# Kernel optimization log

Hardware: AMD Instinct MI355X
Metric: run time of the kernel (lower is better)

Reference implementation:

```python
import jax, jax.numpy as jnp
import numpy as np

N_EMBD = 1024
N_HEAD = 16
HEAD_DIM = N_EMBD // N_HEAD
B, T = 2, 2048
EPS = 1e-5


def _layernorm(x, gamma, beta):
    mu = jnp.mean(x, axis=-1, keepdims=True)
    var = jnp.mean((x - mu) ** 2, axis=-1, keepdims=True)
    return gamma * (x - mu) / jnp.sqrt(var + EPS) + beta


def setup_inputs() -> dict:
    key = jax.random.key(0)
    ks = jax.random.split(key, 12)
    s = 0.02
    d, f = N_EMBD, 4 * N_EMBD
    return {
        "x": jax.random.normal(ks[0], (B, T, d), dtype=jnp.float32),
        "ln1_g": jnp.ones((d,), jnp.float32),
        "ln1_b": jnp.zeros((d,), jnp.float32),
        "wq": jax.random.normal(ks[1], (d, d), jnp.float32) * s,
        "bq": jnp.zeros((d,), jnp.float32),
        "wk": jax.random.normal(ks[2], (d, d), jnp.float32) * s,
        "bk": jnp.zeros((d,), jnp.float32),
        "wv": jax.random.normal(ks[3], (d, d), jnp.float32) * s,
        "bv": jnp.zeros((d,), jnp.float32),
        "wo": jax.random.normal(ks[4], (d, d), jnp.float32) * s,
        "bo": jnp.zeros((d,), jnp.float32),
        "ln2_g": jnp.ones((d,), jnp.float32),
        "ln2_b": jnp.zeros((d,), jnp.float32),
        "w1": jax.random.normal(ks[5], (d, f), jnp.float32) * s,
        "b1": jnp.zeros((f,), jnp.float32),
        "w2": jax.random.normal(ks[6], (f, d), jnp.float32) * s,
        "b2": jnp.zeros((d,), jnp.float32),
    }


def reference(x, ln1_g, ln1_b, wq, bq, wk, bk, wv, bv, wo, bo,
              ln2_g, ln2_b, w1, b1, w2, b2):
    Bn, Tn, C = x.shape
    # --- attention branch (dropout = identity, eval mode) ---
    xn = _layernorm(x, ln1_g, ln1_b)
    q = (xn @ wq + bq).reshape(Bn, Tn, N_HEAD, HEAD_DIM)
    k = (xn @ wk + bk).reshape(Bn, Tn, N_HEAD, HEAD_DIM)
    v = (xn @ wv + bv).reshape(Bn, Tn, N_HEAD, HEAD_DIM)
    scale = 1.0 / jnp.sqrt(jnp.float32(HEAD_DIM))
    scores = jnp.einsum("bqhd,bkhd->bhqk", q, k) * scale  # [B,H,T,T]
    causal = jnp.tril(jnp.ones((Tn, Tn), dtype=bool))
    scores = jnp.where(causal[None, None], scores, -jnp.inf)
    weights = jax.nn.softmax(scores, axis=-1)
    attn = jnp.einsum("bhqk,bkhd->bqhd", weights, v).reshape(Bn, Tn, C)
    x = x + (attn @ wo + bo)
    # --- MLP branch ---
    h = _layernorm(x, ln2_g, ln2_b)
    h = jax.nn.gelu(h @ w1 + b1, approximate=False)
    x = x + (h @ w2 + b2)
    return x
```

## Files before the change

### kernel.cpp

```cpp
#include <hip/hip_runtime.h>
#include <stdint.h>

#define T_SEQ 2048
#define NHEAD 16
#define HDIM 64
#define CDIM 1024
#define FDIM 4096
#define MROWS 4096
#define NQB 32
#define SMAX 8.0f

typedef __bf16 bf16;
typedef __bf16 bf16x8 __attribute__((ext_vector_type(8)));
typedef float f32x4 __attribute__((ext_vector_type(4)));

__device__ __forceinline__ void gload_lds16(const void* g, void* l) {
  __builtin_amdgcn_global_load_lds(
      (const __attribute__((address_space(1))) void*)g,
      (__attribute__((address_space(3))) void*)l, 16, 0, 0);
}

__device__ __forceinline__ float gelu_tanh(float v) {
  float u = 0.7978845608f * (v + 0.044715f * v * v * v);
  float e = exp2f(u * 2.885390082f);
  float th = 1.0f - 2.0f / (e + 1.0f);
  return 0.5f * v * (1.0f + th);
}

__device__ __forceinline__ void wt_body(const float* __restrict__ src,
                                        bf16* __restrict__ dst, int K, int N,
                                        int k0, int n0) {
  __shared__ float tile[64][65];
  int tid = threadIdx.x;
  int r4 = tid >> 4, c4 = (tid & 15) * 4;
#pragma unroll
  for (int p = 0; p < 4; ++p) {
    int r = p * 16 + r4;
    float4 v = *(const float4*)&src[(size_t)(k0 + r) * N + n0 + c4];
    tile[r][c4] = v.x; tile[r][c4 + 1] = v.y;
    tile[r][c4 + 2] = v.z; tile[r][c4 + 3] = v.w;
  }
  __syncthreads();
  int n8 = tid >> 3, k8 = (tid & 7) * 8;
#pragma unroll
  for (int p = 0; p < 2; ++p) {
    int n = p * 32 + n8;
    union { bf16 h[8]; uint4 u; } t;
#pragma unroll
    for (int j = 0; j < 8; ++j) t.h[j] = (bf16)tile[k8 + j][n];
    *(uint4*)&dst[(size_t)(n0 + n) * K + k0 + k8] = t.u;
  }
}

__global__ void wt_kernel(const float* __restrict__ src, bf16* __restrict__ dst,
                          int K, int N) {
  wt_body(src, dst, K, N, blockIdx.y * 64, blockIdx.x * 64);
}

__global__ void wt4_kernel(const float* s0, const float* s1, const float* s2,
                           const float* s3, bf16* d0, bf16* d1, bf16* d2, bf16* d3) {
  const float* src = blockIdx.z == 0 ? s0 : blockIdx.z == 1 ? s1 : blockIdx.z == 2 ? s2 : s3;
  bf16* dst = blockIdx.z == 0 ? d0 : blockIdx.z == 1 ? d1 : blockIdx.z == 2 ? d2 : d3;
  wt_body(src, dst, 1024, 1024, blockIdx.y * 64, blockIdx.x * 64);
}

__global__ void vt_kernel(const bf16* __restrict__ v, bf16* __restrict__ vt) {
  __shared__ bf16 tile[64][65];
  int bh = blockIdx.y;
  int t0 = blockIdx.x * 64;
  int tid = threadIdx.x;
  const bf16* src = v + (size_t)bh * T_SEQ * HDIM;
  bf16* dst = vt + (size_t)bh * HDIM * T_SEQ;
  int r8 = tid >> 3, c8 = (tid & 7) * 8;
#pragma unroll
  for (int p = 0; p < 2; ++p) {
    int r = p * 32 + r8;
    union { uint4 u; bf16 h[8]; } t;
    t.u = *(const uint4*)&src[(size_t)(t0 + r) * HDIM + c8];
#pragma unroll
    for (int j = 0; j < 8; ++j) tile[r][c8 + j] = t.h[j];
  }
  __syncthreads();
#pragma unroll
  for (int p = 0; p < 2; ++p) {
    int d = p * 32 + r8;
    union { uint4 u; bf16 h[8]; } t;
#pragma unroll
    for (int j = 0; j < 8; ++j) t.h[j] = tile[c8 + j][d];
    *(uint4*)&dst[(size_t)d * T_SEQ + t0 + c8] = t.u;
  }
}

__global__ __launch_bounds__(256)
void ln_kernel(const float* __restrict__ x, const float* __restrict__ g,
               const float* __restrict__ b, bf16* __restrict__ out) {
  int row = blockIdx.x;
  int tid = threadIdx.x;
  float4 v = *(const float4*)&x[(size_t)row * CDIM + tid * 4];
  float s = v.x + v.y + v.z + v.w;
  float ss = v.x * v.x + v.y * v.y + v.z * v.z + v.w * v.w;
#pragma unroll
  for (int off = 1; off < 64; off <<= 1) {
    s += __shfl_xor(s, off, 64);
    ss += __shfl_xor(ss, off, 64);
  }
  __shared__ float red[8];
  int wv = tid >> 6, ln = tid & 63;
  if (ln == 0) { red[wv] = s; red[4 + wv] = ss; }
  __syncthreads();
  s = red[0] + red[1] + red[2] + red[3];
  ss = red[4] + red[5] + red[6] + red[7];
  float mu = s * (1.0f / CDIM);
  float var = ss * (1.0f / CDIM) - mu * mu;
  float rstd = rsqrtf(var + 1e-5f);
  float4 gv = *(const float4*)&g[tid * 4];
  float4 bv = *(const float4*)&b[tid * 4];
  union { bf16 h[4]; uint2 u; } o;
  o.h[0] = (bf16)(gv.x * (v.x - mu) * rstd + bv.x);
  o.h[1] = (bf16)(gv.y * (v.y - mu) * rstd + bv.y);
  o.h[2] = (bf16)(gv.z * (v.z - mu) * rstd + bv.z);
  o.h[3] = (bf16)(gv.w * (v.w - mu) * rstd + bv.w);
  *(uint2*)&out[(size_t)row * CDIM + tid * 4] = o.u;
}

__global__ __launch_bounds__(256)
void addp_kernel(float* __restrict__ out, const float* __restrict__ p1, int n4) {
  int i = blockIdx.x * 256 + threadIdx.x;
  int stride = gridDim.x * 256;
  for (; i < n4; i += stride) {
    f32x4 a = *(const f32x4*)&out[i * 4];
    f32x4 b = *(const f32x4*)&p1[i * 4];
    a += b;
    *(f32x4*)&out[i * 4] = a;
  }
}

enum { EPI_QKV = 0, EPI_F32RES = 1, EPI_GELU = 2, EPI_SPLIT = 3 };

template <int EPI, int BN>
__global__ __launch_bounds__(512, 1)
void gemm256(const bf16* __restrict__ A, const bf16* __restrict__ Bt,
             const float* __restrict__ bias, const float* __restrict__ bias2,
             const float* __restrict__ bias3, const float* res,
             void* outp, void* out2, void* out3, int M, int N, int K, int Kstride) {
  constexpr int WCOLS = BN / 64;
  constexpr int WROWS = 8 / WCOLS;
  constexpr int MR = (256 / WROWS) / 16;
  constexpr int MH = MR / 2;
  constexpr int BCH = BN / 128;
  __shared__ __align__(16) bf16 As[3][256 * 32];
  __shared__ __align__(16) bf16 Bs[3][BN * 32];
  int tid = threadIdx.x;
  int w = tid >> 6, l = tid & 63;
  int wr = w / WCOLS, wc = w % WCOLS;
  int lo = l & 15, g = l >> 4;

  int nwg = gridDim.x * gridDim.y;
  int orig = blockIdx.y * gridDim.x + blockIdx.x;
  int lid = (orig & 7) * (nwg >> 3) + (orig >> 3);
  int bx = lid % gridDim.x, by = lid / gridDim.x;
  int m0 = by * 256, n0 = bx * BN;
  int koff = blockIdx.z * K;

  f32x4 acc[MR][4];
#pragma unroll
  for (int i = 0; i < MR; ++i)
#pragma unroll
    for (int j = 0; j < 4; ++j) acc[i][j] = (f32x4){0.f, 0.f, 0.f, 0.f};

  const bf16* Ab = A + (size_t)m0 * Kstride + koff;
  const bf16* Bb = Bt + (size_t)n0 * Kstride + koff;

  int srow = tid >> 2;
  int scol = ((tid & 3) ^ ((tid >> 3) & 3)) * 8;
  auto STAGE_A = [&](int t, int buf) {
    int k0 = t * 32;
#pragma unroll
    for (int c = 0; c < 2; ++c)
      gload_lds16(Ab + (size_t)(c * 128 + srow) * Kstride + k0 + scol,
                  &As[buf][c * 4096 + w * 512]);
  };
  auto STAGE_B = [&](int t, int buf) {
    int k0 = t * 32;
#pragma unroll
    for (int c = 0; c < BCH; ++c)
      gload_lds16(Bb + (size_t)(c * 128 + srow) * Kstride + k0 + scol,
                  &Bs[buf][c * 4096 + w * 512]);
  };

  int nt = K >> 5;
  STAGE_A(0, 0); STAGE_B(0, 0);
  STAGE_A(1, 1); STAGE_B(1, 1);
  if constexpr (BN == 256) asm volatile("s_waitcnt vmcnt(4)" ::: "memory");
  else                     asm volatile("s_waitcnt vmcnt(3)" ::: "memory");
  __syncthreads();
  int sw = (lo >> 1) & 3;
  int b0 = 0;
  for (int t = 0; t < nt; ++t) {
    int b2 = b0 - 1; if (b2 < 0) b2 += 3;
    bf16x8 af[MH], bfr[4];
#pragma unroll
    for (int m = 0; m < MH; ++m) {
      int R = wr * (MR * 16) + m * 16 + lo;
      af[m] = *(const bf16x8*)&As[b0][R * 32 + (g ^ sw) * 8];
    }
#pragma unroll
    for (int n = 0; n < 4; ++n) {
      int R = wc * 64 + n * 16 + lo;
      bfr[n] = *(const bf16x8*)&Bs[b0][R * 32 + (g ^ sw) * 8];
    }
    if (t + 2 < nt) STAGE_A(t + 2, b2);
    asm volatile("s_barrier" ::: "memory");
    __builtin_amdgcn_s_setprio(1);
#pragma unroll
    for (int m = 0; m < MH; ++m)
#pragma unroll
      for (int n = 0; n < 4; ++n)
        acc[m][n] = __builtin_amdgcn_mfma_f32_16x16x32_bf16(af[m], bfr[n], acc[m][n], 0, 0, 0);
    __builtin_amdgcn_s_setprio(0);
#pragma unroll
    for (int m = 0; m < MH; ++m) {
      int R = wr * (MR * 16) + (m + MH) * 16 + lo;
      af[m] = *(const bf16x8*)&As[b0][R * 32 + (g ^ sw) * 8];
    }
    if (t + 2 < nt) {
      STAGE_B(t + 2, b2);
      if constexpr (BN == 256) asm volatile("s_waitcnt vmcnt(4)" ::: "memory");
      else                     asm volatile("s_waitcnt vmcnt(3)" ::: "memory");
    } else if (t + 1 < nt) {
      asm volatile("s_waitcnt vmcnt(0)" ::: "memory");
    }
    asm volatile("s_barrier" ::: "memory");
    __builtin_amdgcn_s_setprio(1);
#pragma unroll
    for (int m = 0; m < MH; ++m)
#pragma unroll
      for (int n = 0; n < 4; ++n)
        acc[m + MH][n] = __builtin_amdgcn_mfma_f32_16x16x32_bf16(af[m], bfr[n], acc[m + MH][n], 0, 0, 0);
    __builtin_amdgcn_s_setprio(0);
    b0 = (b0 == 2) ? 0 : b0 + 1;
  }

  if constexpr (EPI == EPI_QKV) {
    int which = n0 >> 10;
    const float* bb = which == 0 ? bias : (which == 1 ? bias2 : bias3);
    bf16* ob = (bf16*)(which == 0 ? outp : (which == 1 ? out2 : out3));
#pragma unroll
    for (int m = 0; m < MR; ++m)
#pragma unroll
      for (int n = 0; n < 4; ++n)
#pragma unroll
        for (int j = 0; j < 4; ++j) {
          int row = m0 + wr * (MR * 16) + m * 16 + g * 4 + j;
          int col = n0 + wc * 64 + n * 16 + lo;
          int cw = col & (CDIM - 1);
          float v = acc[m][n][j] + bb[cw];
          int b = row >> 11, tt = row & (T_SEQ - 1);
          int h = cw >> 6, d = cw & (HDIM - 1);
          ob[(((size_t)(b * NHEAD + h)) * T_SEQ + tt) * HDIM + d] = (bf16)v;
        }
  } else if constexpr (EPI == EPI_SPLIT) {
#pragma unroll
    for (int m = 0; m < MR; ++m)
#pragma unroll
      for (int n = 0; n < 4; ++n)
#pragma unroll
        for (int j = 0; j < 4; ++j) {
          int row = m0 + wr * (MR * 16) + m * 16 + g * 4 + j;
          int col = n0 + wc * 64 + n * 16 + lo;
          if (blockIdx.z == 0) {
            float v = acc[m][n][j] + bias[col];
            ((float*)outp)[(size_t)row * N + col] = v + res[(size_t)row * N + col];
          } else {
            ((float*)out2)[(size_t)row * N + col] = acc[m][n][j];
          }
        }
  } else {
#pragma unroll
    for (int m = 0; m < MR; ++m)
#pragma unroll
      for (int n = 0; n < 4; ++n)
#pragma unroll
        for (int j = 0; j < 4; ++j) {
          int row = m0 + wr * (MR * 16) + m * 16 + g * 4 + j;
          int col = n0 + wc * 64 + n * 16 + lo;
          float v = acc[m][n][j] + bias[col];
          if constexpr (EPI == EPI_F32RES) {
            ((float*)outp)[(size_t)row * N + col] = v + res[(size_t)row * N + col];
          } else {
            ((bf16*)outp)[(size_t)row * N + col] = (bf16)gelu_tanh(v);
          }
        }
  }
}

template <int EPI, int TN>
__global__ __launch_bounds__(256, 2)
void gemm_bt(const bf16* __restrict__ A, const bf16* __restrict__ Bt,
             const float* __restrict__ bias, const float* __restrict__ bias2,
             const float* __restrict__ bias3, const float* res,
             void* outp, void* out2, void* out3, int M, int N, int K, int Kstride) {
  constexpr int MR = (TN == 128) ? 4 : 2;
  __shared__ __align__(16) bf16 As[4][128 * 32];
  __shared__ __align__(16) bf16 Bs[4][TN * 32];
  int tid = threadIdx.x;
  int w = tid >> 6, l = tid & 63;
  int lo = l & 15, g = l >> 4;
  int rowb = (TN == 128) ? (w >> 1) * 64 : w * 32;
  int colb = (TN == 128) ? (w & 1) * 64 : 0;

  int nwg = gridDim.x * gridDim.y;
  int orig = blockIdx.y * gridDim.x + blockIdx.x;
  int lid = (orig & 7) * (nwg >> 3) + (orig >> 3);
  int bx = lid % gridDim.x, by = lid / gridDim.x;
  int m0 = by * 128, n0 = bx * TN;

  f32x4 acc[MR][4];
#pragma unroll
  for (int i = 0; i < MR; ++i)
#pragma unroll
    for (int j = 0; j < 4; ++j) acc[i][j] = (f32x4){0.f, 0.f, 0.f, 0.f};

  const bf16* Ab = A + (size_t)m0 * Kstride;
  const bf16* Bb = Bt + (size_t)n0 * Kstride;

  auto STAGE = [&](int t, int buf) {
    int k0 = t * 32;
    int row = (l >> 2);
    int col = ((l & 3) ^ ((l >> 3) & 3)) * 8;
#pragma unroll
    for (int i = 0; i < 2; ++i) {
      int c = w * 2 + i;
      gload_lds16(Ab + (size_t)(c * 16 + row) * Kstride + k0 + col, &As[buf][c * 512]);
    }
    if constexpr (TN == 128) {
#pragma unroll
      for (int i = 0; i < 2; ++i) {
        int c = w * 2 + i;
        gload_lds16(Bb + (size_t)(c * 16 + row) * Kstride + k0 + col, &Bs[buf][c * 512]);
      }
    } else {
      int c = w;
      gload_lds16(Bb + (size_t)(c * 16 + row) * Kstride + k0 + col, &Bs[buf][c * 512]);
    }
  };

  int nt = K >> 5;
  STAGE(0, 0);
  STAGE(1, 1);
  STAGE(2, 2);
  int sw = (lo >> 1) & 3;
  for (int t = 0; t < nt; ++t) {
    if constexpr (TN == 128) {
      if (t + 2 < nt)      asm volatile("s_waitcnt vmcnt(8)" ::: "memory");
      else if (t + 1 < nt) asm volatile("s_waitcnt vmcnt(4)" ::: "memory");
      else                 asm volatile("s_waitcnt vmcnt(0)" ::: "memory");
    } else {
      if (t + 2 < nt)      asm volatile("s_waitcnt vmcnt(6)" ::: "memory");
      else if (t + 1 < nt) asm volatile("s_waitcnt vmcnt(3)" ::: "memory");
      else                 asm volatile("s_waitcnt vmcnt(0)" ::: "memory");
    }
    __builtin_amdgcn_s_barrier();
    __builtin_amdgcn_sched_barrier(0);
    int cur = t & 3;
    bf16x8 af[MR], bfr[4];
#pragma unroll
    for (int m = 0; m < MR; ++m) {
      int R = rowb + m * 16 + lo;
      af[m] = *(const bf16x8*)&As[cur][R * 32 + (g ^ sw) * 8];
    }
#pragma unroll
    for (int n = 0; n < 4; ++n) {
      int R = colb + n * 16 + lo;
      bfr[n] = *(const bf16x8*)&Bs[cur][R * 32 + (g ^ sw) * 8];
    }
    if (t + 3 < nt) STAGE(t + 3, (t + 3) & 3);
    __builtin_amdgcn_s_setprio(1);
#pragma unroll
    for (int m = 0; m < MR; ++m)
#pragma unroll
      for (int n = 0; n < 4; ++n)
        acc[m][n] = __builtin_amdgcn_mfma_f32_16x16x32_bf16(af[m], bfr[n], acc[m][n], 0, 0, 0);
    __builtin_amdgcn_s_setprio(0);
  }

#pragma unroll
  for (int m = 0; m < MR; ++m)
#pragma unroll
    for (int n = 0; n < 4; ++n)
#pragma unroll
      for (int j = 0; j < 4; ++j) {
        int row = m0 + rowb + m * 16 + g * 4 + j;
        int col = n0 + colb + n * 16 + lo;
        float v = acc[m][n][j] + bias[col];
        if constexpr (EPI == EPI_F32RES) {
          ((float*)outp)[(size_t)row * N + col] = v + res[(size_t)row * N + col];
        } else {
          ((bf16*)outp)[(size_t)row * N + col] = (bf16)gelu_tanh(v);
        }
      }
}

__device__ __forceinline__ void attn_tile(
    const bf16* __restrict__ Ksb, const bf16* __restrict__ Vsb,
    const bf16x8 qf[2], f32x4 Ot[4],
    float& lsum, int lo, int g, int kbase, int myq, bool diag) {
  bf16x8 vf[2][4];
#pragma unroll
  for (int ks = 0; ks < 2; ++ks)
#pragma unroll
    for (int dt = 0; dt < 4; ++dt) {
      int R = dt * 16 + lo;
      int slot = (ks * 4 + g) ^ (R & 7);
      vf[ks][dt] = *(const bf16x8*)&Vsb[R * 64 + slot * 8];
    }
  f32x4 st[4];
  int fs = (lo & 3) | (((lo >> 2) & 1) << 2);
#pragma unroll
  for (int kt = 0; kt < 4; ++kt) {
    f32x4 a = (f32x4){0.f, 0.f, 0.f, 0.f};
    int R = (kt >> 1) * 32 + ((lo >> 2) * 8) + (kt & 1) * 4 + (lo & 3);
#pragma unroll
    for (int dh = 0; dh < 2; ++dh) {
      int slot = (dh * 4 + g) ^ fs;
      bf16x8 kf = *(const bf16x8*)&Ksb[R * 64 + slot * 8];
      a = __builtin_amdgcn_mfma_f32_16x16x32_bf16(kf, qf[dh], a, 0, 0, 0);
    }
    st[kt] = a;
  }
  if (diag) {
#pragma unroll
    for (int kt = 0; kt < 4; ++kt)
#pragma unroll
      for (int j = 0; j < 4; ++j) {
        int key = kbase + (kt >> 1) * 32 + g * 8 + (kt & 1) * 4 + j;
        if (key > myq) st[kt][j] = -1e30f;
      }
  }
  float csum = 0.f;
  union { bf16 h[8]; bf16x8 v8; } pf[2];
#pragma unroll
  for (int kt = 0; kt < 4; ++kt)
#pragma unroll
    for (int j = 0; j < 4; ++j) {
      float pv = exp2f(st[kt][j] - SMAX);
      csum += pv;
      pf[kt >> 1].h[(kt & 1) * 4 + j] = (bf16)pv;
    }
  lsum += csum;
#pragma unroll
  for (int ks = 0; ks < 2; ++ks)
#pragma unroll
    for (int dt = 0; dt < 4; ++dt)
      Ot[dt] = __builtin_amdgcn_mfma_f32_16x16x32_bf16(vf[ks][dt], pf[ks].v8, Ot[dt], 0, 0, 0);
}

__global__ __launch_bounds__(256, 2)
void attn_kernel(const bf16* __restrict__ q, const bf16* __restrict__ k,
                 const bf16* __restrict__ vt, bf16* __restrict__ out) {
  __shared__ __align__(16) bf16 Ks[2][64 * 64];
  __shared__ __align__(16) bf16 Vs[2][64 * 64];
  int tid = threadIdx.x;
  int w = tid >> 6, l = tid & 63;
  int lo = l & 15, g = l >> 4;
  int nwg = gridDim.x * gridDim.y;
  int orig = blockIdx.y * gridDim.x + blockIdx.x;
  int lid = (orig & 7) * (nwg >> 3) + (orig >> 3);
  int p = lid & 15;
  int bh = lid >> 4;
  int qA = p, qB = NQB - 1 - p;
  int nch = qB + 1;
  const bf16* qh = q + (size_t)bh * T_SEQ * HDIM;
  const bf16* kh = k + (size_t)bh * T_SEQ * HDIM;
  const bf16* vh = vt + (size_t)bh * HDIM * T_SEQ;

  const float sc = 0.125f * 1.44269504f;
  bf16x8 qfA[2], qfB[2];
#pragma unroll
  for (int dh = 0; dh < 2; ++dh) {
    bf16x8 tA = *(const bf16x8*)&qh[(size_t)(qA * 64 + w * 16 + lo) * HDIM + dh * 32 + g * 8];
    bf16x8 tB = *(const bf16x8*)&qh[(size_t)(qB * 64 + w * 16 + lo) * HDIM + dh * 32 + g * 8];
#pragma unroll
    for (int j = 0; j < 8; ++j) {
      qfA[dh][j] = (bf16)((float)tA[j] * sc);
      qfB[dh][j] = (bf16)((float)tB[j] * sc);
    }
  }
  int myqA = qA * 64 + w * 16 + lo;
  int myqB = qB * 64 + w * 16 + lo;

  f32x4 OtA[4], OtB[4];
#pragma unroll
  for (int i = 0; i < 4; ++i) {
    OtA[i] = (f32x4){0.f, 0.f, 0.f, 0.f};
    OtB[i] = (f32x4){0.f, 0.f, 0.f, 0.f};
  }
  float lA = 0.f, lB = 0.f;

  int srow8 = l >> 3, s0 = l & 7;
  auto STAGE = [&](int kc, int buf) {
#pragma unroll
    for (int i = 0; i < 2; ++i) {
      int c = w * 2 + i;
      int r = c * 8 + srow8;
      int ek = (s0 ^ ((r & 3) | (((r >> 3) & 1) << 2))) * 8;
      int ev = (s0 ^ (r & 7)) * 8;
      gload_lds16(&kh[(size_t)(kc * 64 + r) * HDIM + ek], &Ks[buf][c * 512]);
      gload_lds16(&vh[(size_t)r * T_SEQ + kc * 64 + ev], &Vs[buf][c * 512]);
    }
  };

  STAGE(0, 0);
  int cur = 0;
  for (int kc = 0; kc < nch; ++kc) {
    __syncthreads();
    if (kc + 1 < nch) STAGE(kc + 1, cur ^ 1);
    attn_tile(Ks[cur], Vs[cur], qfB, OtB, lB, lo, g, kc * 64, myqB,
              kc == nch - 1);
    if (kc <= p)
      attn_tile(Ks[cur], Vs[cur], qfA, OtA, lA, lo, g, kc * 64, myqA,
                kc == p);
    cur ^= 1;
  }

  lA += __shfl_xor(lA, 16, 64);
  lA += __shfl_xor(lA, 32, 64);
  lB += __shfl_xor(lB, 16, 64);
  lB += __shfl_xor(lB, 32, 64);

  int b = bh >> 4, h = bh & 15;
  {
    float inv = 1.0f / lA;
    bf16* ob = out + (((size_t)b * T_SEQ + myqA) * NHEAD + h) * HDIM;
#pragma unroll
    for (int dt = 0; dt < 4; ++dt)
#pragma unroll
      for (int j = 0; j < 4; ++j) ob[dt * 16 + g * 4 + j] = (bf16)(OtA[dt][j] * inv);
  }
  {
    float inv = 1.0f / lB;
    bf16* ob = out + (((size_t)b * T_SEQ + myqB) * NHEAD + h) * HDIM;
#pragma unroll
    for (int dt = 0; dt < 4; ++dt)
#pragma unroll
      for (int j = 0; j < 4; ++j) ob[dt * 16 + g * 4 + j] = (bf16)(OtB[dt][j] * inv);
  }
}

extern "C" void kernel_launch(void* const* d_in, const int* in_sizes, int n_in,
                              void* d_out, int out_size, void* d_ws, size_t ws_size,
                              hipStream_t stream) {
  (void)in_sizes; (void)n_in; (void)out_size; (void)ws_size;
  const float* x     = (const float*)d_in[0];
  const float* ln1_g = (const float*)d_in[1];
  const float* ln1_b = (const float*)d_in[2];
  const float* wq    = (const float*)d_in[3];
  const float* bq    = (const float*)d_in[4];
  const float* wk    = (const float*)d_in[5];
  const float* bk    = (const float*)d_in[6];
  const float* wv    = (const float*)d_in[7];
  const float* bv    = (const float*)d_in[8];
  const float* wo    = (const float*)d_in[9];
  const float* bo    = (const float*)d_in[10];
  const float* ln2_g = (const float*)d_in[11];
  const float* ln2_b = (const float*)d_in[12];
  const float* w1    = (const float*)d_in[13];
  const float* b1    = (const float*)d_in[14];
  const float* w2    = (const float*)d_in[15];
  const float* b2    = (const float*)d_in[16];
  float* out = (float*)d_out;

  const size_t MB = 1024ull * 1024ull;
  char* ws = (char*)d_ws;
  bf16* wqkvT = (bf16*)(ws + 0 * MB);
  bf16* wqT = wqkvT;
  bf16* wkT = (bf16*)(ws + 2 * MB);
  bf16* wvT = (bf16*)(ws + 4 * MB);
  bf16* woT = (bf16*)(ws + 6 * MB);
  bf16* w1T = (bf16*)(ws + 8 * MB);
  bf16* w2T = (bf16*)(ws + 16 * MB);
  bf16* xn  = (bf16*)(ws + 24 * MB);
  bf16* qb_ = (bf16*)(ws + 32 * MB);
  bf16* kb_ = (bf16*)(ws + 40 * MB);
  bf16* vb_ = (bf16*)(ws + 48 * MB);
  bf16* vtb = (bf16*)(ws + 56 * MB);
  bf16* aout = (bf16*)(ws + 24 * MB);
  bf16* hn  = (bf16*)(ws + 32 * MB);
  bf16* hb  = (bf16*)(ws + 40 * MB);
  float* p1 = (float*)(ws + 24 * MB);

  dim3 blk(256);
  wt4_kernel<<<dim3(16, 16, 4), blk, 0, stream>>>(wq, wk, wv, wo, wqT, wkT, wvT, woT);
  wt_kernel<<<dim3(64, 16), blk, 0, stream>>>(w1, w1T, 1024, 4096);
  wt_kernel<<<dim3(16, 64), blk, 0, stream>>>(w2, w2T, 4096, 1024);

  ln_kernel<<<MROWS, blk, 0, stream>>>(x, ln1_g, ln1_b, xn);

  gemm256<EPI_QKV, 256><<<dim3(12, 16), dim3(512), 0, stream>>>(
      xn, wqkvT, bq, bk, bv, nullptr, qb_, kb_, vb_, MROWS, 3 * CDIM, CDIM, CDIM);

  vt_kernel<<<dim3(32, 32), blk, 0, stream>>>(vb_, vtb);
  attn_kernel<<<dim3(16, 32), blk, 0, stream>>>(qb_, kb_, vtb, aout);

  gemm_bt<EPI_F32RES, 64><<<dim3(16, 32), blk, 0, stream>>>(
      aout, woT, bo, nullptr, nullptr, x, out, nullptr, nullptr, MROWS, CDIM, CDIM, CDIM);

  ln_kernel<<<MROWS, blk, 0, stream>>>(out, ln2_g, ln2_b, hn);

  gemm256<EPI_GELU, 256><<<dim3(16, 16), dim3(512), 0, stream>>>(
      hn, w1T, b1, nullptr, nullptr, nullptr, hb, nullptr, nullptr, MROWS, FDIM, CDIM, CDIM);

  gemm256<EPI_SPLIT, 128><<<dim3(8, 16, 2), dim3(512), 0, stream>>>(
      hb, w2T, b2, nullptr, nullptr, out, out, p1, nullptr, MROWS, CDIM, FDIM / 2, FDIM);
  addp_kernel<<<2048, blk, 0, stream>>>(out, p1, MROWS * CDIM / 4);
}
```

Baseline: 228.9 us.

## Replace split-K partial buffer and add kernel with atomic accumulation into output

The final MLP down-projection GEMM now splits K four ways with 256-wide tiles and accumulates every split directly into the residual output using float atomicAdd. Only the first split adds the bias. This removes the separate fp32 partial buffer and the extra add kernel launch along with its memory traffic. In exchange it issues scalar atomics for every output element, and the summation order is no longer deterministic. The residual is added implicitly, since out already holds x plus the attention branch.

```diff
diff --git a/kernel.cpp b/kernel.cpp
--- a/kernel.cpp
+++ b/kernel.cpp
@@ -123,19 +123,7 @@
   *(uint2*)&out[(size_t)row * CDIM + tid * 4] = o.u;
 }
 
-__global__ __launch_bounds__(256)
-void addp_kernel(float* __restrict__ out, const float* __restrict__ p1, int n4) {
-  int i = blockIdx.x * 256 + threadIdx.x;
-  int stride = gridDim.x * 256;
-  for (; i < n4; i += stride) {
-    f32x4 a = *(const f32x4*)&out[i * 4];
-    f32x4 b = *(const f32x4*)&p1[i * 4];
-    a += b;
-    *(f32x4*)&out[i * 4] = a;
-  }
-}
-
-enum { EPI_QKV = 0, EPI_F32RES = 1, EPI_GELU = 2, EPI_SPLIT = 3 };
+enum { EPI_QKV = 0, EPI_F32RES = 1, EPI_GELU = 2, EPI_ATOM = 3 };
 
 template <int EPI, int BN>
 __global__ __launch_bounds__(512, 1)
@@ -259,7 +247,9 @@
           int h = cw >> 6, d = cw & (HDIM - 1);
           ob[(((size_t)(b * NHEAD + h)) * T_SEQ + tt) * HDIM + d] = (bf16)v;
         }
-  } else if constexpr (EPI == EPI_SPLIT) {
+  } else if constexpr (EPI == EPI_ATOM) {
+    float* op = (float*)outp;
+    bool z0 = (blockIdx.z == 0);
 #pragma unroll
     for (int m = 0; m < MR; ++m)
 #pragma unroll
@@ -268,12 +258,8 @@
         for (int j = 0; j < 4; ++j) {
           int row = m0 + wr * (MR * 16) + m * 16 + g * 4 + j;
           int col = n0 + wc * 64 + n * 16 + lo;
-          if (blockIdx.z == 0) {
-            float v = acc[m][n][j] + bias[col];
-            ((float*)outp)[(size_t)row * N + col] = v + res[(size_t)row * N + col];
-          } else {
-            ((float*)out2)[(size_t)row * N + col] = acc[m][n][j];
-          }
+          float v = acc[m][n][j] + (z0 ? bias[col] : 0.0f);
+          atomicAdd(&op[(size_t)row * N + col], v);
         }
   } else {
 #pragma unroll
@@ -587,7 +573,6 @@
   bf16* aout = (bf16*)(ws + 24 * MB);
   bf16* hn  = (bf16*)(ws + 32 * MB);
   bf16* hb  = (bf16*)(ws + 40 * MB);
-  float* p1 = (float*)(ws + 24 * MB);
 
   dim3 blk(256);
   wt4_kernel<<<dim3(16, 16, 4), blk, 0, stream>>>(wq, wk, wv, wo, wqT, wkT, wvT, woT);
@@ -610,7 +595,7 @@
   gemm256<EPI_GELU, 256><<<dim3(16, 16), dim3(512), 0, stream>>>(
       hn, w1T, b1, nullptr, nullptr, nullptr, hb, nullptr, nullptr, MROWS, FDIM, CDIM, CDIM);
 
-  gemm256<EPI_SPLIT, 128><<<dim3(8, 16, 2), dim3(512), 0, stream>>>(
-      hb, w2T, b2, nullptr, nullptr, out, out, p1, nullptr, MROWS, CDIM, FDIM / 2, FDIM);
-  addp_kernel<<<2048, blk, 0, stream>>>(out, p1, MROWS * CDIM / 4);
-}
+  gemm256<EPI_ATOM, 256><<<dim3(4, 16, 4), dim3(512), 0, stream>>>(
+      hb, w2T, b2, nullptr, nullptr, nullptr, out, nullptr, nullptr,
+      MROWS, CDIM, FDIM / 4, FDIM);
+}
```

After: 258.7 us. 1.13x slower.

## Use 4-way split-K with bf16 partials and 256-wide tiles for MLP down-projection

Applied to the files above, without the earlier changes.

The second MLP GEMM now splits K four ways with BN=256 tiles (4x16x4 = 256 workgroups) instead of two ways with BN=128. Three of the partial sums are stored as bf16 rather than fp32, and a reduction kernel adds all three into the output. The aim is better CU occupancy, more reuse per tile and less partial-sum traffic. The cost is bf16 rounding of the partial sums, which loses precision, plus reuse of workspace regions (including the woT area) as scratch.

```diff
diff --git a/kernel.cpp b/kernel.cpp
--- a/kernel.cpp
+++ b/kernel.cpp
@@ -124,25 +124,32 @@
 }
 
 __global__ __launch_bounds__(256)
-void addp_kernel(float* __restrict__ out, const float* __restrict__ p1, int n4) {
+void addp3_kernel(float* __restrict__ out, const bf16* __restrict__ p1,
+                  const bf16* __restrict__ p2, const bf16* __restrict__ p3, int n4) {
   int i = blockIdx.x * 256 + threadIdx.x;
   int stride = gridDim.x * 256;
   for (; i < n4; i += stride) {
     f32x4 a = *(const f32x4*)&out[i * 4];
-    f32x4 b = *(const f32x4*)&p1[i * 4];
-    a += b;
+    union { uint2 u; bf16 h[4]; } t1, t2, t3;
+    t1.u = *(const uint2*)&p1[i * 4];
+    t2.u = *(const uint2*)&p2[i * 4];
+    t3.u = *(const uint2*)&p3[i * 4];
+#pragma unroll
+    for (int j = 0; j < 4; ++j)
+      a[j] += (float)t1.h[j] + (float)t2.h[j] + (float)t3.h[j];
     *(f32x4*)&out[i * 4] = a;
   }
 }
 
-enum { EPI_QKV = 0, EPI_F32RES = 1, EPI_GELU = 2, EPI_SPLIT = 3 };
+enum { EPI_QKV = 0, EPI_F32RES = 1, EPI_GELU = 2, EPI_SPLITB = 3 };
 
 template <int EPI, int BN>
 __global__ __launch_bounds__(512, 1)
 void gemm256(const bf16* __restrict__ A, const bf16* __restrict__ Bt,
              const float* __restrict__ bias, const float* __restrict__ bias2,
              const float* __restrict__ bias3, const float* res,
-             void* outp, void* out2, void* out3, int M, int N, int K, int Kstride) {
+             void* outp, void* out2, void* out3, void* out4,
+             int M, int N, int K, int Kstride) {
   constexpr int WCOLS = BN / 64;
   constexpr int WROWS = 8 / WCOLS;
   constexpr int MR = (256 / WROWS) / 16;
@@ -259,22 +266,33 @@
           int h = cw >> 6, d = cw & (HDIM - 1);
           ob[(((size_t)(b * NHEAD + h)) * T_SEQ + tt) * HDIM + d] = (bf16)v;
         }
-  } else if constexpr (EPI == EPI_SPLIT) {
-#pragma unroll
-    for (int m = 0; m < MR; ++m)
-#pragma unroll
-      for (int n = 0; n < 4; ++n)
-#pragma unroll
-        for (int j = 0; j < 4; ++j) {
-          int row = m0 + wr * (MR * 16) + m * 16 + g * 4 + j;
-          int col = n0 + wc * 64 + n * 16 + lo;
-          if (blockIdx.z == 0) {
-            float v = acc[m][n][j] + bias[col];
-            ((float*)outp)[(size_t)row * N + col] = v + res[(size_t)row * N + col];
-          } else {
-            ((float*)out2)[(size_t)row * N + col] = acc[m][n][j];
+  } else if constexpr (EPI == EPI_SPLITB) {
+    if (blockIdx.z == 0) {
+      float* op = (float*)outp;
+#pragma unroll
+      for (int m = 0; m < MR; ++m)
+#pragma unroll
+        for (int n = 0; n < 4; ++n)
+#pragma unroll
+          for (int j = 0; j < 4; ++j) {
+            int row = m0 + wr * (MR * 16) + m * 16 + g * 4 + j;
+            int col = n0 + wc * 64 + n * 16 + lo;
+            size_t idx = (size_t)row * N + col;
+            op[idx] = acc[m][n][j] + bias[col] + op[idx];
           }
-        }
+    } else {
+      bf16* pp = (bf16*)(blockIdx.z == 1 ? out2 : (blockIdx.z == 2 ? out3 : out4));
+#pragma unroll
+      for (int m = 0; m < MR; ++m)
+#pragma unroll
+        for (int n = 0; n < 4; ++n)
+#pragma unroll
+          for (int j = 0; j < 4; ++j) {
+            int row = m0 + wr * (MR * 16) + m * 16 + g * 4 + j;
+            int col = n0 + wc * 64 + n * 16 + lo;
+            pp[(size_t)row * N + col] = (bf16)acc[m][n][j];
+          }
+    }
   } else {
 #pragma unroll
     for (int m = 0; m < MR; ++m)
@@ -587,7 +605,9 @@
   bf16* aout = (bf16*)(ws + 24 * MB);
   bf16* hn  = (bf16*)(ws + 32 * MB);
   bf16* hb  = (bf16*)(ws + 40 * MB);
-  float* p1 = (float*)(ws + 24 * MB);
+  bf16* p1b = (bf16*)(ws + 24 * MB);
+  bf16* p2b = (bf16*)(ws + 32 * MB);
+  bf16* p3b = (bf16*)(ws + 6 * MB);
 
   dim3 blk(256);
   wt4_kernel<<<dim3(16, 16, 4), blk, 0, stream>>>(wq, wk, wv, wo, wqT, wkT, wvT, woT);
@@ -597,7 +617,7 @@
   ln_kernel<<<MROWS, blk, 0, stream>>>(x, ln1_g, ln1_b, xn);
 
   gemm256<EPI_QKV, 256><<<dim3(12, 16), dim3(512), 0, stream>>>(
-      xn, wqkvT, bq, bk, bv, nullptr, qb_, kb_, vb_, MROWS, 3 * CDIM, CDIM, CDIM);
+      xn, wqkvT, bq, bk, bv, nullptr, qb_, kb_, vb_, nullptr, MROWS, 3 * CDIM, CDIM, CDIM);
 
   vt_kernel<<<dim3(32, 32), blk, 0, stream>>>(vb_, vtb);
   attn_kernel<<<dim3(16, 32), blk, 0, stream>>>(qb_, kb_, vtb, aout);
@@ -608,9 +628,11 @@
   ln_kernel<<<MROWS, blk, 0, stream>>>(out, ln2_g, ln2_b, hn);
 
   gemm256<EPI_GELU, 256><<<dim3(16, 16), dim3(512), 0, stream>>>(
-      hn, w1T, b1, nullptr, nullptr, nullptr, hb, nullptr, nullptr, MROWS, FDIM, CDIM, CDIM);
-
-  gemm256<EPI_SPLIT, 128><<<dim3(8, 16, 2), dim3(512), 0, stream>>>(
-      hb, w2T, b2, nullptr, nullptr, out, out, p1, nullptr, MROWS, CDIM, FDIM / 2, FDIM);
-  addp_kernel<<<2048, blk, 0, stream>>>(out, p1, MROWS * CDIM / 4);
-}
+      hn, w1T, b1, nullptr, nullptr, nullptr, hb, nullptr, nullptr, nullptr,
+      MROWS, FDIM, CDIM, CDIM);
+
+  gemm256<EPI_SPLITB, 256><<<dim3(4, 16, 4), dim3(512), 0, stream>>>(
+      hb, w2T, b2, nullptr, nullptr, nullptr, out, p1b, p2b, p3b,
+      MROWS, CDIM, FDIM / 4, FDIM);
+  addp3_kernel<<<2048, blk, 0, stream>>>(out, p1b, p2b, p3b, MROWS * CDIM / 4);
+}
```

Measured after the change: 233.9 us. 1.02x slower.

## Add 128x256-tile triple-buffered GEMM kernel for the MLP projections

Applied to the files above, without the earlier changes.

Adds a new gemm128 kernel with 128x256 output tiles, 64-wide K steps, triple-buffered direct-to-LDS loads and an XOR swizzle. It replaces gemm256 for the two MLP GEMMs (the GELU up-projection and the split-K down-projection). Grids change so more workgroups run: 512 instead of 256 for the up-projection, and 256 instead of 256 with a different tile shape for the down-projection. The split epilogue now reads the residual through the output pointer in place. The aim is better occupancy and latency hiding across CUs, at the cost of more LDS per block (144KB) and one workgroup per CU.

```diff
diff --git a/kernel.cpp b/kernel.cpp
--- a/kernel.cpp
+++ b/kernel.cpp
@@ -259,22 +259,6 @@
           int h = cw >> 6, d = cw & (HDIM - 1);
           ob[(((size_t)(b * NHEAD + h)) * T_SEQ + tt) * HDIM + d] = (bf16)v;
         }
-  } else if constexpr (EPI == EPI_SPLIT) {
-#pragma unroll
-    for (int m = 0; m < MR; ++m)
-#pragma unroll
-      for (int n = 0; n < 4; ++n)
-#pragma unroll
-        for (int j = 0; j < 4; ++j) {
-          int row = m0 + wr * (MR * 16) + m * 16 + g * 4 + j;
-          int col = n0 + wc * 64 + n * 16 + lo;
-          if (blockIdx.z == 0) {
-            float v = acc[m][n][j] + bias[col];
-            ((float*)outp)[(size_t)row * N + col] = v + res[(size_t)row * N + col];
-          } else {
-            ((float*)out2)[(size_t)row * N + col] = acc[m][n][j];
-          }
-        }
   } else {
 #pragma unroll
     for (int m = 0; m < MR; ++m)
@@ -292,6 +276,113 @@
           }
         }
   }
+}
+
+template <int EPI>
+__global__ __launch_bounds__(512, 1)
+void gemm128(const bf16* __restrict__ A, const bf16* __restrict__ Bt,
+             const float* __restrict__ bias, const float* res,
+             void* outp, void* out2, int M, int N, int K, int Kstride) {
+  __shared__ __align__(16) bf16 As[3][128 * 64];
+  __shared__ __align__(16) bf16 Bs[3][256 * 64];
+  int tid = threadIdx.x;
+  int w = tid >> 6, l = tid & 63;
+  int wr = w >> 2, wc = w & 3;
+  int lo = l & 15, g = l >> 4;
+
+  int nwg = gridDim.x * gridDim.y;
+  int orig = blockIdx.y * gridDim.x + blockIdx.x;
+  int lid = (orig & 7) * (nwg >> 3) + (orig >> 3);
+  int bx = lid % gridDim.x, by = lid / gridDim.x;
+  int m0 = by * 128, n0 = bx * 256;
+  int koff = blockIdx.z * K;
+
+  f32x4 acc[4][4];
+#pragma unroll
+  for (int i = 0; i < 4; ++i)
+#pragma unroll
+    for (int j = 0; j < 4; ++j) acc[i][j] = (f32x4){0.f, 0.f, 0.f, 0.f};
+
+  const bf16* Ab = A + (size_t)m0 * Kstride + koff;
+  const bf16* Bb = Bt + (size_t)n0 * Kstride + koff;
+
+  int sr = l >> 3;
+  int sc = ((l & 7) ^ sr) * 8;
+  auto STAGE = [&](int t, int buf) {
+    int k0 = t * 64;
+#pragma unroll
+    for (int L = 0; L < 2; ++L)
+      gload_lds16(Ab + (size_t)(L * 64 + w * 8 + sr) * Kstride + k0 + sc,
+                  &As[buf][(L * 64 + w * 8) * 64]);
+#pragma unroll
+    for (int L = 0; L < 4; ++L)
+      gload_lds16(Bb + (size_t)(L * 64 + w * 8 + sr) * Kstride + k0 + sc,
+                  &Bs[buf][(L * 64 + w * 8) * 64]);
+  };
+
+  int nt = K >> 6;
+  STAGE(0, 0);
+  STAGE(1, 1);
+  int rsl = lo & 7;
+  for (int t = 0; t < nt; ++t) {
+    int buf = t % 3;
+    if (t + 1 < nt) asm volatile("s_waitcnt vmcnt(6)" ::: "memory");
+    else            asm volatile("s_waitcnt vmcnt(0)" ::: "memory");
+    __builtin_amdgcn_s_barrier();
+    __builtin_amdgcn_sched_barrier(0);
+    bf16x8 af[4], bf4[4];
+    int s0 = (g ^ rsl) * 8;
+#pragma unroll
+    for (int m = 0; m < 4; ++m)
+      af[m] = *(const bf16x8*)&As[buf][(wr * 64 + m * 16 + lo) * 64 + s0];
+#pragma unroll
+    for (int n = 0; n < 4; ++n)
+      bf4[n] = *(const bf16x8*)&Bs[buf][(wc * 64 + n * 16 + lo) * 64 + s0];
+    if (t + 2 < nt) STAGE(t + 2, (t + 2) % 3);
+    __builtin_amdgcn_s_setprio(1);
+#pragma unroll
+    for (int m = 0; m < 4; ++m)
+#pragma unroll
+      for (int n = 0; n < 4; ++n)
+        acc[m][n] = __builtin_amdgcn_mfma_f32_16x16x32_bf16(af[m], bf4[n], acc[m][n], 0, 0, 0);
+    __builtin_amdgcn_s_setprio(0);
+    int s1 = ((4 + g) ^ rsl) * 8;
+#pragma unroll
+    for (int m = 0; m < 4; ++m)
+      af[m] = *(const bf16x8*)&As[buf][(wr * 64 + m * 16 + lo) * 64 + s1];
+#pragma unroll
+    for (int n = 0; n < 4; ++n)
+      bf4[n] = *(const bf16x8*)&Bs[buf][(wc * 64 + n * 16 + lo) * 64 + s1];
+    __builtin_amdgcn_s_setprio(1);
+#pragma unroll
+    for (int m = 0; m < 4; ++m)
+#pragma unroll
+      for (int n = 0; n < 4; ++n)
+        acc[m][n] = __builtin_amdgcn_mfma_f32_16x16x32_bf16(af[m], bf4[n], acc[m][n], 0, 0, 0);
+    __builtin_amdgcn_s_setprio(0);
+  }
+
+#pragma unroll
+  for (int m = 0; m < 4; ++m)
+#pragma unroll
+    for (int n = 0; n < 4; ++n)
+#pragma unroll
+      for (int j = 0; j < 4; ++j) {
+        int row = m0 + wr * 64 + m * 16 + g * 4 + j;
+        int col = n0 + wc * 64 + n * 16 + lo;
+        if constexpr (EPI == EPI_GELU) {
+          float v = acc[m][n][j] + bias[col];
+          ((bf16*)outp)[(size_t)row * N + col] = (bf16)gelu_tanh(v);
+        } else {
+          size_t idx = (size_t)row * N + col;
+          if (blockIdx.z == 0) {
+            float* op = (float*)outp;
+            op[idx] = acc[m][n][j] + bias[col] + op[idx];
+          } else {
+            ((float*)out2)[idx] = acc[m][n][j];
+          }
+        }
+      }
 }
 
 template <int EPI, int TN>
@@ -607,10 +698,10 @@
 
   ln_kernel<<<MROWS, blk, 0, stream>>>(out, ln2_g, ln2_b, hn);
 
-  gemm256<EPI_GELU, 256><<<dim3(16, 16), dim3(512), 0, stream>>>(
-      hn, w1T, b1, nullptr, nullptr, nullptr, hb, nullptr, nullptr, MROWS, FDIM, CDIM, CDIM);
-
-  gemm256<EPI_SPLIT, 128><<<dim3(8, 16, 2), dim3(512), 0, stream>>>(
-      hb, w2T, b2, nullptr, nullptr, out, out, p1, nullptr, MROWS, CDIM, FDIM / 2, FDIM);
+  gemm128<EPI_GELU><<<dim3(16, 32), dim3(512), 0, stream>>>(
+      hn, w1T, b1, nullptr, hb, nullptr, MROWS, FDIM, CDIM, CDIM);
+
+  gemm128<EPI_SPLIT><<<dim3(4, 32, 2), dim3(512), 0, stream>>>(
+      hb, w2T, b2, nullptr, out, p1, MROWS, CDIM, FDIM / 2, FDIM);
   addp_kernel<<<2048, blk, 0, stream>>>(out, p1, MROWS * CDIM / 4);
 }
```

Measured after the change: 242.3 us. 1.06x slower.
